# Optimization experiments

Hardware: AMD Instinct MI355X
Metric: run time of the kernel (lower is better)

Reference implementation:

```python
import jax, jax.numpy as jnp
import numpy as np

H, D_NOPE, D_ROPE, D_V, L_KV, HID = 16, 128, 64, 128, 512, 2048
D_QK = D_NOPE + D_ROPE
THETA = 10000.0
EPS = 1e-6


def _rope(x, positions):
    # neox-style rotary over last dim (D_ROPE); x: [T, ..., D_ROPE]
    half = D_ROPE // 2
    inv_freq = 1.0 / (THETA ** (jnp.arange(half, dtype=jnp.float32) * 2.0 / D_ROPE))
    ang = positions.astype(jnp.float32)[:, None] * inv_freq[None, :]  # [T, half]
    shape = (x.shape[0],) + (1,) * (x.ndim - 2) + (half,)
    cos, sin = jnp.cos(ang).reshape(shape), jnp.sin(ang).reshape(shape)
    x1, x2 = x[..., :half], x[..., half:]
    return jnp.concatenate([x1 * cos - x2 * sin, x2 * cos + x1 * sin], axis=-1)


def _rmsnorm(x, w):
    var = jnp.mean(x * x, axis=-1, keepdims=True)
    return x * jax.lax.rsqrt(var + EPS) * w


def setup_inputs() -> dict:
    key = jax.random.key(0)
    ks = jax.random.split(key, 6)
    T = 4096
    s = lambda fan_in: 1.0 / np.sqrt(fan_in)
    return {
        "positions": jnp.arange(T, dtype=jnp.int32),
        "hidden_states": jax.random.normal(ks[0], (T, HID), jnp.float32),
        "Wq": jax.random.normal(ks[1], (HID, H * D_QK), jnp.float32) * s(HID),
        "Wkva": jax.random.normal(ks[2], (HID, L_KV + D_ROPE), jnp.float32) * s(HID),
        "kv_a_ln_w": jnp.ones((L_KV,), jnp.float32),
        "Wkvb": jax.random.normal(ks[3], (L_KV, H * (D_NOPE + D_V)), jnp.float32) * s(L_KV),
        "Wo": jax.random.normal(ks[4], (H * D_V, HID), jnp.float32) * s(H * D_V),
    }


def reference(positions, hidden_states, Wq, Wkva, kv_a_ln_w, Wkvb, Wo):
    T = hidden_states.shape[0]
    scaling = 1.0 / np.sqrt(D_QK)

    q = (hidden_states @ Wq).reshape(T, H, D_QK)
    q_nope, q_pe = q[..., :D_NOPE], q[..., D_NOPE:]

    latent = hidden_states @ Wkva                    # [T, L_KV + D_ROPE]
    kv_a = _rmsnorm(latent[:, :L_KV], kv_a_ln_w)     # [T, L_KV]
    k_pe = latent[:, L_KV:]                          # [T, D_ROPE] (shared across heads)

    kv = (kv_a @ Wkvb).reshape(T, H, D_NOPE + D_V)
    k_nope, v = kv[..., :D_NOPE], kv[..., D_NOPE:]

    q_pe = _rope(q_pe, positions)                    # [T, H, D_ROPE]
    k_pe = _rope(k_pe, positions)                    # [T, D_ROPE]

    q = jnp.concatenate([q_nope, q_pe], axis=-1)     # [T, H, D_QK]
    k = jnp.concatenate(
        [k_nope, jnp.broadcast_to(k_pe[:, None, :], (T, H, D_ROPE))], axis=-1)

    scores = jnp.einsum("thd,shd->hts", q, k) * scaling        # [H, T, T]
    causal = positions[:, None] >= positions[None, :]           # [T, T]
    scores = jnp.where(causal[None], scores, jnp.finfo(scores.dtype).min)
    attn = jax.nn.softmax(scores, axis=-1)
    out = jnp.einsum("hts,shd->thd", attn, v)                   # [T, H, D_V]
    return out.reshape(T, H * D_V) @ Wo                          # [T, HID]
```

## Files before the change

kernel.cpp:

```cpp
#include <hip/hip_runtime.h>
#include <hip/hip_bf16.h>

#define T_LEN 4096
#define HID_DIM 2048
#define NH 16
#define DNOPE 128
#define DROPE 64
#define DV 128
#define LKV 512
#define DQK 192

#define BN 64

typedef __attribute__((ext_vector_type(8))) __bf16 bf16x8;
typedef __attribute__((ext_vector_type(4))) float f32x4;
typedef __attribute__((ext_vector_type(4))) short s16x4;

__device__ __forceinline__ unsigned short f2b(float f) {
  unsigned u = __builtin_bit_cast(unsigned, f);
  unsigned r = (u + 0x7FFFu + ((u >> 16) & 1u)) >> 16;
  return (unsigned short)r;
}

#define GL2LDS16(gp, lp)                                                   \
  __builtin_amdgcn_global_load_lds(                                        \
      (const __attribute__((address_space(1))) unsigned int*)(gp),         \
      (__attribute__((address_space(3))) unsigned int*)(lp), 16, 0, 0)

#if __has_builtin(__builtin_amdgcn_mfma_f32_16x16x16bf16_1k)
#define HAVE_MFMA16 1
__device__ __forceinline__ f32x4 mfma16(s16x4 a, s16x4 b, f32x4 c) {
  return __builtin_amdgcn_mfma_f32_16x16x16bf16_1k(a, b, c, 0, 0, 0);
}
#elif __has_builtin(__builtin_amdgcn_mfma_f32_16x16x16_bf16)
#define HAVE_MFMA16 1
typedef __attribute__((ext_vector_type(4))) __bf16 bf16x4v;
__device__ __forceinline__ f32x4 mfma16(s16x4 a, s16x4 b, f32x4 c) {
  return __builtin_amdgcn_mfma_f32_16x16x16_bf16(
      __builtin_bit_cast(bf16x4v, a), __builtin_bit_cast(bf16x4v, b), c, 0, 0, 0);
}
#else
#define HAVE_MFMA16 0
#endif

__global__ void k_cvt(const float* __restrict__ in, unsigned short* __restrict__ out, int n) {
  int i = blockIdx.x * 256 + threadIdx.x;
  if (i < n) out[i] = f2b(in[i]);
}

__global__ void k_transpose_all(const float* __restrict__ Wq, const float* __restrict__ Wkva,
                                const float* __restrict__ Wkvb, const float* __restrict__ Wo,
                                unsigned short* __restrict__ WqT, unsigned short* __restrict__ WkvaT,
                                unsigned short* __restrict__ WkvbT, unsigned short* __restrict__ WoT) {
  __shared__ float t[32][33];
  int bid = blockIdx.x;
  const float* in; unsigned short* out; int R, C, bx, by;
  if (bid < 6144)      { in = Wq;   out = WqT;   R = 2048; C = 3072; bx = bid % 96;  by = bid / 96; }
  else if (bid < 7296) { int b = bid - 6144; in = Wkva; out = WkvaT; R = 2048; C = 576;  bx = b % 18;  by = b / 18; }
  else if (bid < 9344) { int b = bid - 7296; in = Wkvb; out = WkvbT; R = 512;  C = 4096; bx = b % 128; by = b / 128; }
  else                 { int b = bid - 9344; in = Wo;   out = WoT;   R = 2048; C = 2048; bx = b % 64;  by = b / 64; }
  int c0 = bx * 32, r0 = by * 32;
  int tx = threadIdx.x, ty = threadIdx.y;
#pragma unroll
  for (int k = 0; k < 4; k++)
    t[ty + 8 * k][tx] = in[(size_t)(r0 + ty + 8 * k) * C + c0 + tx];
  __syncthreads();
#pragma unroll
  for (int k = 0; k < 4; k++)
    out[(size_t)(c0 + ty + 8 * k) * R + r0 + tx] = f2b(t[tx][ty + 8 * k]);
}

#define GEMM_CORE(Aptr, Btptr, Nn, Kk, ldaa, ldbb)                                         \
  __shared__ unsigned short As[128 * 32];                                                  \
  __shared__ unsigned short Bs[128 * 32];                                                  \
  int tid = threadIdx.x;                                                                   \
  int lane = tid & 63, w = tid >> 6;                                                       \
  int quad = lane >> 4, l16 = lane & 15;                                                   \
  int wm = (w >> 1) * 64, wn = (w & 1) * 64;                                               \
  int i0 = tid, i1 = tid + 256;                                                            \
  int rA0 = i0 >> 2, rA1 = i1 >> 2;                                                        \
  int c80 = (i0 & 3) * 8, c81 = (i1 & 3) * 8;                                              \
  const unsigned short* Ag0 = (Aptr) + (size_t)(m0 + rA0) * (ldaa) + c80;                  \
  const unsigned short* Ag1 = (Aptr) + (size_t)(m0 + rA1) * (ldaa) + c81;                  \
  int bR0 = n0 + rA0; if (bR0 >= (Nn)) bR0 = (Nn) - 1;                                     \
  int bR1 = n0 + rA1; if (bR1 >= (Nn)) bR1 = (Nn) - 1;                                     \
  const unsigned short* Bg0 = (Btptr) + (size_t)bR0 * (ldbb) + c80;                        \
  const unsigned short* Bg1 = (Btptr) + (size_t)bR1 * (ldbb) + c81;                        \
  f32x4 acc[4][4] = {};                                                                    \
  for (int k0 = 0; k0 < (Kk); k0 += 32) {                                                  \
    GL2LDS16(Ag0 + k0, &As[i0 * 8]);                                                       \
    GL2LDS16(Ag1 + k0, &As[i1 * 8]);                                                       \
    GL2LDS16(Bg0 + k0, &Bs[i0 * 8]);                                                       \
    GL2LDS16(Bg1 + k0, &Bs[i1 * 8]);                                                       \
    __syncthreads();                                                                       \
    bf16x8 aF[4], bF[4];                                                                   \
    _Pragma("unroll")                                                                      \
    for (int i = 0; i < 4; i++)                                                            \
      aF[i] = *(const bf16x8*)&As[(wm + i * 16 + l16) * 32 + quad * 8];                    \
    _Pragma("unroll")                                                                      \
    for (int j = 0; j < 4; j++)                                                            \
      bF[j] = *(const bf16x8*)&Bs[(wn + j * 16 + l16) * 32 + quad * 8];                    \
    _Pragma("unroll")                                                                      \
    for (int i = 0; i < 4; i++)                                                            \
      _Pragma("unroll")                                                                    \
      for (int j = 0; j < 4; j++)                                                          \
        acc[i][j] = __builtin_amdgcn_mfma_f32_16x16x32_bf16(aF[i], bF[j], acc[i][j], 0, 0, 0); \
    __syncthreads();                                                                       \
  }                                                                                        \
  int row0 = m0 + wm + quad * 4; (void)row0;

__global__ __launch_bounds__(256) void k_gemm128(
    const unsigned short* __restrict__ A, const unsigned short* __restrict__ Bt,
    float* __restrict__ Cf, int N, int K, int lda, int ldb, int ldc) {
  int m0 = blockIdx.y * 128, n0 = blockIdx.x * 128;
  GEMM_CORE(A, Bt, N, K, lda, ldb)
#pragma unroll
  for (int i = 0; i < 4; i++)
#pragma unroll
    for (int j = 0; j < 4; j++) {
      int col = n0 + wn + j * 16 + l16;
      if (col < N)
#pragma unroll
        for (int r = 0; r < 4; r++)
          Cf[(size_t)(row0 + i * 16 + r) * ldc + col] = acc[i][j][r];
    }
}

__global__ __launch_bounds__(256) void k_gemm_proj(
    const unsigned short* __restrict__ A, const unsigned short* __restrict__ WqT,
    const unsigned short* __restrict__ WkvaT, const int* __restrict__ pos,
    unsigned short* __restrict__ Qh, float* __restrict__ latentf) {
  int bxx = blockIdx.x;
  bool iswq = bxx < 24;
  const unsigned short* Bt = iswq ? WqT : WkvaT;
  int N = iswq ? NH * DQK : (LKV + DROPE);
  int m0 = blockIdx.y * 128, n0 = (iswq ? bxx : bxx - 24) * 128;
  GEMM_CORE(A, Bt, N, HID_DIM, HID_DIM, HID_DIM)
  if (iswq) {
    const float scale = 0.07216878364870323f;
    int b64 = (n0 + wn) >> 6;
    int h = b64 / 3, rem3 = b64 - 3 * h;
    unsigned short* Qb = Qh + (size_t)h * T_LEN * DQK;
    if (rem3 < 2) {
#pragma unroll
      for (int i = 0; i < 4; i++)
#pragma unroll
        for (int r = 0; r < 4; r++) {
          int t = row0 + i * 16 + r;
#pragma unroll
          for (int j = 0; j < 4; j++)
            Qb[(size_t)t * DQK + rem3 * 64 + j * 16 + l16] = f2b(acc[i][j][r] * scale);
        }
    } else {
#pragma unroll
      for (int i = 0; i < 4; i++)
#pragma unroll
        for (int r = 0; r < 4; r++) {
          int t = row0 + i * 16 + r;
          float p = (float)pos[t];
#pragma unroll
          for (int j = 0; j < 2; j++) {
            int idx = j * 16 + l16;
            float inv = __expf((float)idx * -0.2878231366242557f);
            float sn, cs;
            __sincosf(p * inv, &sn, &cs);
            float x1 = acc[i][j][r] * scale, x2 = acc[i][j + 2][r] * scale;
            Qb[(size_t)t * DQK + DNOPE + idx]      = f2b(x1 * cs - x2 * sn);
            Qb[(size_t)t * DQK + DNOPE + 32 + idx] = f2b(x2 * cs + x1 * sn);
          }
        }
    }
  } else {
#pragma unroll
    for (int i = 0; i < 4; i++)
#pragma unroll
      for (int j = 0; j < 4; j++) {
        int col = n0 + wn + j * 16 + l16;
        if (col < LKV + DROPE)
#pragma unroll
          for (int r = 0; r < 4; r++)
            latentf[(size_t)(row0 + i * 16 + r) * (LKV + DROPE) + col] = acc[i][j][r];
      }
  }
}

__global__ __launch_bounds__(256) void k_gemm_wkvb(
    const unsigned short* __restrict__ A, const unsigned short* __restrict__ Bt,
    unsigned short* __restrict__ Kh, unsigned short* __restrict__ VT) {
  int m0 = blockIdx.y * 128, n0 = blockIdx.x * 128;
  GEMM_CORE(A, Bt, NH * 256, LKV, LKV, LKV)
#pragma unroll
  for (int i = 0; i < 4; i++)
#pragma unroll
    for (int j = 0; j < 4; j++) {
      int col = n0 + wn + j * 16 + l16;
      int h = col >> 8, c = col & 255;
#pragma unroll
      for (int r = 0; r < 4; r++) {
        int t = row0 + i * 16 + r;
        unsigned short v = f2b(acc[i][j][r]);
        if (c < 128) Kh[((size_t)h * T_LEN + t) * DQK + c] = v;
        else         VT[((size_t)(h * 128 + c - 128)) * T_LEN + t] = v;
      }
    }
}

__global__ __launch_bounds__(256) void k_prep_latent(
    const float* __restrict__ latent, const float* __restrict__ w,
    const int* __restrict__ pos,
    unsigned short* __restrict__ kva, unsigned short* __restrict__ Kh) {
  __shared__ float red[256];
  int t = blockIdx.x;
  const float* row = latent + (size_t)t * (LKV + DROPE);
  float ss = 0.f;
  for (int c = threadIdx.x; c < LKV; c += 256) { float v = row[c]; ss += v * v; }
  red[threadIdx.x] = ss;
  __syncthreads();
  for (int s = 128; s > 0; s >>= 1) {
    if (threadIdx.x < s) red[threadIdx.x] += red[threadIdx.x + s];
    __syncthreads();
  }
  float rs = rsqrtf(red[0] / (float)LKV + 1e-6f);
  for (int c = threadIdx.x; c < LKV; c += 256)
    kva[(size_t)t * LKV + c] = f2b(row[c] * rs * w[c]);
  if (threadIdx.x < DROPE) {
    int i = threadIdx.x;
    float p = (float)pos[t];
    float val;
    if (i < 32) {
      float x1 = row[LKV + i], x2 = row[LKV + i + 32];
      float inv = __expf(-(float)i * 0.2878231366242557f);
      float sn, cs; __sincosf(p * inv, &sn, &cs);
      val = x1 * cs - x2 * sn;
    } else {
      float x1 = row[LKV + i - 32], x2 = row[LKV + i];
      float inv = __expf(-(float)(i - 32) * 0.2878231366242557f);
      float sn, cs; __sincosf(p * inv, &sn, &cs);
      val = x2 * cs + x1 * sn;
    }
    unsigned short vb = f2b(val);
#pragma unroll
    for (int h = 0; h < NH; h++)
      Kh[((size_t)h * T_LEN + t) * DQK + DNOPE + i] = vb;
  }
}

__global__ __launch_bounds__(256, 2) void k_flash(
    const unsigned short* __restrict__ Qh, const unsigned short* __restrict__ Kh,
    const unsigned short* __restrict__ VT, unsigned short* __restrict__ attn) {
  int bx = blockIdx.x;
  int h = bx & 15;
  int t = (bx & 255) >> 4;
  int qb = (bx < 256) ? (31 - t) : t;
  int m0 = qb * 128;
  int diagA = 2 * qb, diagB = 2 * qb + 1;
  int NT = 2 * qb + 2;

  __shared__ unsigned short Ks[64 * 24 * 8];
  __shared__ unsigned short Vs[128 * 8 * 8];

  int tid = threadIdx.x, lane = tid & 63, w = tid >> 6;
  int quad = lane >> 4, l16 = lane & 15;
  int x = l16 & 7;

  const unsigned short* Qbase = Qh + (size_t)h * T_LEN * DQK;
  const unsigned short* Kbase = Kh + (size_t)h * T_LEN * DQK;
  const unsigned short* Vbase = VT + (size_t)h * DV * T_LEN;

  bf16x8 qfS[6], qfL[6];
#pragma unroll
  for (int kk = 0; kk < 6; kk++) {
    qfS[kk] = *(const bf16x8*)(Qbase + (size_t)(m0 + w * 16 + l16) * DQK + kk * 32 + quad * 8);
    qfL[kk] = *(const bf16x8*)(Qbase + (size_t)(m0 + 64 + w * 16 + l16) * DQK + kk * 32 + quad * 8);
  }

  int koff[6], voff[4];
#pragma unroll
  for (int k = 0; k < 6; k++) {
    int c = tid + k * 256;
    int row = c / 24, sc = c - row * 24;
    int cg = (sc & 0x18) | ((sc ^ row) & 7);
    koff[k] = row * DQK + cg * 8;
  }
#pragma unroll
  for (int k = 0; k < 4; k++) {
    int c = tid + k * 256;
    int row = c >> 3, sc = c & 7;
    int cg = sc ^ (row & 7);
    voff[k] = row * T_LEN + cg * 8;
  }

  int kEo[4], kOo[4], vAo[4];
#pragma unroll
  for (int st = 0; st < 4; st++) {
    int rb = (st * 16 + l16) * 192;
    kEo[st] = rb + ((quad ^ x) * 8);
    kOo[st] = rb + (((quad + 4) ^ x) * 8);
    vAo[st] = l16 * 64 + (((st * 2 + (quad >> 1)) ^ x) * 8) + (quad & 1) * 4;
  }

  f32x4 OaccS[8] = {}, OaccL[8] = {};
  float liS = 0.f, liL = 0.f;
  int mS = m0 + w * 16 + l16;
  int mL = mS + 64;

#if !HAVE_MFMA16
  int lA = l16 + ((quad & 1) << 5);
  int lB = lA + 16;
  bool lowq = (quad < 2);
  int vFo[2];
#pragma unroll
  for (int u = 0; u < 2; u++)
    vFo[u] = l16 * 64 + (((u * 4 + quad) ^ x) * 8);
#endif

  for (int j = 0; j < NT; ++j) {
#pragma unroll
    for (int k = 0; k < 6; k++) GL2LDS16(Kbase + koff[k], &Ks[(tid + k * 256) * 8]);
#pragma unroll
    for (int k = 0; k < 4; k++) GL2LDS16(Vbase + voff[k], &Vs[(tid + k * 256) * 8]);
#pragma unroll
    for (int k = 0; k < 6; k++) koff[k] += BN * DQK;
#pragma unroll
    for (int k = 0; k < 4; k++) voff[k] += BN;
    __syncthreads();

    f32x4 ScS[4] = {}, ScL[4] = {};
#pragma unroll
    for (int kk = 0; kk < 6; kk++) {
#pragma unroll
      for (int st = 0; st < 4; st++) {
        bf16x8 kb = *(const bf16x8*)(Ks + ((kk & 1) ? kOo[st] : kEo[st]) + (kk >> 1) * 64);
        ScS[st] = __builtin_amdgcn_mfma_f32_16x16x32_bf16(kb, qfS[kk], ScS[st], 0, 0, 0);
        ScL[st] = __builtin_amdgcn_mfma_f32_16x16x32_bf16(kb, qfL[kk], ScL[st], 0, 0, 0);
      }
    }

    int n0 = j * BN;
    if (j >= diagA) {
#pragma unroll
      for (int st = 0; st < 4; st++)
#pragma unroll
        for (int r = 0; r < 4; r++) {
          int s = n0 + st * 16 + quad * 4 + r;
          if (s > mS) ScS[st][r] = -1e30f;
        }
    }
    if (j == diagB) {
#pragma unroll
      for (int st = 0; st < 4; st++)
#pragma unroll
        for (int r = 0; r < 4; r++) {
          int s = n0 + st * 16 + quad * 4 + r;
          if (s > mL) ScL[st][r] = -1e30f;
        }
    }

    unsigned p0S[4], p1S[4], p0L[4], p1L[4];
#pragma unroll
    for (int st = 0; st < 4; st++) {
      float e0 = __expf(ScS[st][0]);
      float e1 = __expf(ScS[st][1]);
      float e2 = __expf(ScS[st][2]);
      float e3 = __expf(ScS[st][3]);
      liS += (e0 + e1) + (e2 + e3);
      p0S[st] = __builtin_amdgcn_perm(__builtin_bit_cast(unsigned, e1),
                                      __builtin_bit_cast(unsigned, e0), 0x07060302u);
      p1S[st] = __builtin_amdgcn_perm(__builtin_bit_cast(unsigned, e3),
                                      __builtin_bit_cast(unsigned, e2), 0x07060302u);
      float f0 = __expf(ScL[st][0]);
      float f1 = __expf(ScL[st][1]);
      float f2 = __expf(ScL[st][2]);
      float f3 = __expf(ScL[st][3]);
      liL += (f0 + f1) + (f2 + f3);
      p0L[st] = __builtin_amdgcn_perm(__builtin_bit_cast(unsigned, f1),
                                      __builtin_bit_cast(unsigned, f0), 0x07060302u);
      p1L[st] = __builtin_amdgcn_perm(__builtin_bit_cast(unsigned, f3),
                                      __builtin_bit_cast(unsigned, f2), 0x07060302u);
    }

#if HAVE_MFMA16
#pragma unroll
    for (int st = 0; st < 4; st++) {
      uint2 puS; puS.x = p0S[st]; puS.y = p1S[st];
      s16x4 pbS = __builtin_bit_cast(s16x4, puS);
      uint2 puL; puL.x = p0L[st]; puL.y = p1L[st];
      s16x4 pbL = __builtin_bit_cast(s16x4, puL);
#pragma unroll
      for (int dt = 0; dt < 8; dt++) {
        s16x4 va = __builtin_bit_cast(s16x4, *(const uint2*)(Vs + vAo[st] + dt * 1024));
        OaccS[dt] = mfma16(va, pbS, OaccS[dt]);
        OaccL[dt] = mfma16(va, pbL, OaccL[dt]);
      }
    }
#else
#pragma unroll
    for (int u = 0; u < 2; u++) {
      int a0 = __shfl((int)p0S[2 * u], lA, 64);
      int a1 = __shfl((int)p0S[2 * u + 1], lA, 64);
      int b0 = __shfl((int)p1S[2 * u], lA, 64);
      int b1 = __shfl((int)p1S[2 * u + 1], lA, 64);
      int c0 = __shfl((int)p0S[2 * u], lB, 64);
      int c1 = __shfl((int)p0S[2 * u + 1], lB, 64);
      int d0 = __shfl((int)p1S[2 * u], lB, 64);
      int d1 = __shfl((int)p1S[2 * u + 1], lB, 64);
      int4 pkS;
      pkS.x = lowq ? a0 : a1; pkS.y = lowq ? b0 : b1;
      pkS.z = lowq ? c0 : c1; pkS.w = lowq ? d0 : d1;
      bf16x8 pbS = __builtin_bit_cast(bf16x8, pkS);
      int sa0 = __shfl((int)p0L[2 * u], lA, 64);
      int sa1 = __shfl((int)p0L[2 * u + 1], lA, 64);
      int sb0 = __shfl((int)p1L[2 * u], lA, 64);
      int sb1 = __shfl((int)p1L[2 * u + 1], lA, 64);
      int sc0 = __shfl((int)p0L[2 * u], lB, 64);
      int sc1 = __shfl((int)p0L[2 * u + 1], lB, 64);
      int sd0 = __shfl((int)p1L[2 * u], lB, 64);
      int sd1 = __shfl((int)p1L[2 * u + 1], lB, 64);
      int4 pkL;
      pkL.x = lowq ? sa0 : sa1; pkL.y = lowq ? sb0 : sb1;
      pkL.z = lowq ? sc0 : sc1; pkL.w = lowq ? sd0 : sd1;
      bf16x8 pbL = __builtin_bit_cast(bf16x8, pkL);
#pragma unroll
      for (int dt = 0; dt < 8; dt++) {
        bf16x8 va = *(const bf16x8*)(Vs + vFo[u] + dt * 1024);
        OaccS[dt] = __builtin_amdgcn_mfma_f32_16x16x32_bf16(va, pbS, OaccS[dt], 0, 0, 0);
        OaccL[dt] = __builtin_amdgcn_mfma_f32_16x16x32_bf16(va, pbL, OaccL[dt], 0, 0, 0);
      }
    }
#endif
    __syncthreads();
  }

  liS += __shfl_xor(liS, 16, 64);
  liS += __shfl_xor(liS, 32, 64);
  liL += __shfl_xor(liL, 16, 64);
  liL += __shfl_xor(liL, 32, 64);

  float invS = 1.f / liS;
  float invL = 1.f / liL;
  unsigned short* dstS = attn + (size_t)mS * HID_DIM + h * DV + quad * 4;
  unsigned short* dstL = attn + (size_t)mL * HID_DIM + h * DV + quad * 4;
#pragma unroll
  for (int dt = 0; dt < 8; dt++) {
    unsigned lo = (unsigned)f2b(OaccS[dt][0] * invS) |
                  ((unsigned)f2b(OaccS[dt][1] * invS) << 16);
    unsigned hi = (unsigned)f2b(OaccS[dt][2] * invS) |
                  ((unsigned)f2b(OaccS[dt][3] * invS) << 16);
    uint2 pkv = {lo, hi};
    *(uint2*)(dstS + dt * 16) = pkv;
    unsigned lo2 = (unsigned)f2b(OaccL[dt][0] * invL) |
                   ((unsigned)f2b(OaccL[dt][1] * invL) << 16);
    unsigned hi2 = (unsigned)f2b(OaccL[dt][2] * invL) |
                   ((unsigned)f2b(OaccL[dt][3] * invL) << 16);
    uint2 pkv2 = {lo2, hi2};
    *(uint2*)(dstL + dt * 16) = pkv2;
  }
}

extern "C" void kernel_launch(void* const* d_in, const int* in_sizes, int n_in,
                              void* d_out, int out_size, void* d_ws, size_t ws_size,
                              hipStream_t stream) {
  const int*   positions = (const int*)d_in[0];
  const float* hs   = (const float*)d_in[1];
  const float* Wq   = (const float*)d_in[2];
  const float* Wkva = (const float*)d_in[3];
  const float* lnw  = (const float*)d_in[4];
  const float* Wkvb = (const float*)d_in[5];
  const float* Wo   = (const float*)d_in[6];
  float* out = (float*)d_out;

  char* p = (char*)d_ws;
  size_t off = 0;
  auto alloc = [&](size_t bytes) {
    char* r = p + off;
    off = (off + bytes + 255) & ~(size_t)255;
    return r;
  };
  unsigned short* hsb     = (unsigned short*)alloc((size_t)T_LEN * HID_DIM * 2);
  unsigned short* WqT     = (unsigned short*)alloc((size_t)(NH * DQK) * HID_DIM * 2);
  unsigned short* WkvaT   = (unsigned short*)alloc((size_t)(LKV + DROPE) * HID_DIM * 2);
  unsigned short* WkvbT   = (unsigned short*)alloc((size_t)(NH * 256) * LKV * 2);
  unsigned short* WoT     = (unsigned short*)alloc((size_t)HID_DIM * HID_DIM * 2);
  unsigned short* Qh      = (unsigned short*)alloc((size_t)NH * T_LEN * DQK * 2);
  unsigned short* kva     = (unsigned short*)alloc((size_t)T_LEN * LKV * 2);
  unsigned short* Kh      = (unsigned short*)alloc((size_t)NH * T_LEN * DQK * 2);
  unsigned short* VT      = (unsigned short*)alloc((size_t)NH * DV * T_LEN * 2);
  unsigned short* attn    = (unsigned short*)alloc((size_t)T_LEN * HID_DIM * 2);
  float*          latentf = (float*)alloc((size_t)T_LEN * (LKV + DROPE) * 4);

  k_cvt<<<(T_LEN * HID_DIM + 255) / 256, 256, 0, stream>>>(hs, hsb, T_LEN * HID_DIM);
  k_transpose_all<<<13440, dim3(32, 8), 0, stream>>>(Wq, Wkva, Wkvb, Wo, WqT, WkvaT, WkvbT, WoT);

  k_gemm_proj<<<dim3(29, T_LEN / 128), 256, 0, stream>>>(hsb, WqT, WkvaT, positions, Qh, latentf);

  k_prep_latent<<<T_LEN, 256, 0, stream>>>(latentf, lnw, positions, kva, Kh);

  k_gemm_wkvb<<<dim3((NH * 256) / 128, T_LEN / 128), 256, 0, stream>>>(kva, WkvbT, Kh, VT);

  k_flash<<<dim3(512), 256, 0, stream>>>(Qh, Kh, VT, attn);

  k_gemm128<<<dim3(HID_DIM / 128, T_LEN / 128), 256, 0, stream>>>(
      attn, WoT, out, HID_DIM, HID_DIM, HID_DIM, HID_DIM, HID_DIM);
}
```

Measured before the change: 500.7 us.

## Double-buffer K/V shared-memory tiles in flash attention kernel

Allocates two LDS buffers for the K and V tiles and issues the global-to-LDS loads for the next tile before computing on the current one. The per-iteration pair of barriers becomes one vmcnt wait plus barrier at the end of each iteration. This is meant to hide global load latency behind MFMA work. It doubles LDS use per block, which could limit occupancy if LDS capacity is tight.

New measurement: 499.6 us. About the same (-0.2%).

```diff
diff --git a/kernel.cpp b/kernel.cpp
--- a/kernel.cpp
+++ b/kernel.cpp
@@ -256,8 +256,8 @@
   int diagA = 2 * qb, diagB = 2 * qb + 1;
   int NT = 2 * qb + 2;
 
-  __shared__ unsigned short Ks[64 * 24 * 8];
-  __shared__ unsigned short Vs[128 * 8 * 8];
+  __shared__ unsigned short Ks[2 * 64 * 24 * 8];
+  __shared__ unsigned short Vs[2 * 128 * 8 * 8];
 
   int tid = threadIdx.x, lane = tid & 63, w = tid >> 6;
   int quad = lane >> 4, l16 = lane & 15;
@@ -314,23 +314,43 @@
     vFo[u] = l16 * 64 + (((u * 4 + quad) ^ x) * 8);
 #endif
 
+#define STAGE(buf)                                                                         \
+  do {                                                                                     \
+    unsigned short* ksd = Ks + (buf) * (64 * 24 * 8);                                      \
+    unsigned short* vsd = Vs + (buf) * (128 * 8 * 8);                                      \
+    _Pragma("unroll")                                                                      \
+    for (int k = 0; k < 6; k++) GL2LDS16(Kbase + koff[k], &ksd[(tid + k * 256) * 8]);      \
+    _Pragma("unroll")                                                                      \
+    for (int k = 0; k < 4; k++) GL2LDS16(Vbase + voff[k], &vsd[(tid + k * 256) * 8]);      \
+    _Pragma("unroll")                                                                      \
+    for (int k = 0; k < 6; k++) koff[k] += BN * DQK;                                       \
+    _Pragma("unroll")                                                                      \
+    for (int k = 0; k < 4; k++) voff[k] += BN;                                             \
+  } while (0)
+
+#define PIPE_BARRIER()                                                                     \
+  do {                                                                                     \
+    asm volatile("s_waitcnt vmcnt(0)" ::: "memory");                                       \
+    __builtin_amdgcn_s_barrier();                                                          \
+    __builtin_amdgcn_sched_barrier(0);                                                     \
+  } while (0)
+
+  STAGE(0);
+  PIPE_BARRIER();
+
+  int cur = 0;
   for (int j = 0; j < NT; ++j) {
-#pragma unroll
-    for (int k = 0; k < 6; k++) GL2LDS16(Kbase + koff[k], &Ks[(tid + k * 256) * 8]);
-#pragma unroll
-    for (int k = 0; k < 4; k++) GL2LDS16(Vbase + voff[k], &Vs[(tid + k * 256) * 8]);
-#pragma unroll
-    for (int k = 0; k < 6; k++) koff[k] += BN * DQK;
-#pragma unroll
-    for (int k = 0; k < 4; k++) voff[k] += BN;
-    __syncthreads();
+    if (j + 1 < NT) STAGE(cur ^ 1);
+
+    const unsigned short* KsB = Ks + cur * (64 * 24 * 8);
+    const unsigned short* VsB = Vs + cur * (128 * 8 * 8);
 
     f32x4 ScS[4] = {}, ScL[4] = {};
 #pragma unroll
     for (int kk = 0; kk < 6; kk++) {
 #pragma unroll
       for (int st = 0; st < 4; st++) {
-        bf16x8 kb = *(const bf16x8*)(Ks + ((kk & 1) ? kOo[st] : kEo[st]) + (kk >> 1) * 64);
+        bf16x8 kb = *(const bf16x8*)(KsB + ((kk & 1) ? kOo[st] : kEo[st]) + (kk >> 1) * 64);
         ScS[st] = __builtin_amdgcn_mfma_f32_16x16x32_bf16(kb, qfS[kk], ScS[st], 0, 0, 0);
         ScL[st] = __builtin_amdgcn_mfma_f32_16x16x32_bf16(kb, qfL[kk], ScL[st], 0, 0, 0);
       }
@@ -388,7 +408,7 @@
       s16x4 pbL = __builtin_bit_cast(s16x4, puL);
 #pragma unroll
       for (int dt = 0; dt < 8; dt++) {
-        s16x4 va = __builtin_bit_cast(s16x4, *(const uint2*)(Vs + vAo[st] + dt * 1024));
+        s16x4 va = __builtin_bit_cast(s16x4, *(const uint2*)(VsB + vAo[st] + dt * 1024));
         OaccS[dt] = mfma16(va, pbS, OaccS[dt]);
         OaccL[dt] = mfma16(va, pbL, OaccL[dt]);
       }
@@ -422,13 +442,15 @@
       bf16x8 pbL = __builtin_bit_cast(bf16x8, pkL);
 #pragma unroll
       for (int dt = 0; dt < 8; dt++) {
-        bf16x8 va = *(const bf16x8*)(Vs + vFo[u] + dt * 1024);
+        bf16x8 va = *(const bf16x8*)(VsB + vFo[u] + dt * 1024);
         OaccS[dt] = __builtin_amdgcn_mfma_f32_16x16x32_bf16(va, pbS, OaccS[dt], 0, 0, 0);
         OaccL[dt] = __builtin_amdgcn_mfma_f32_16x16x32_bf16(va, pbL, OaccL[dt], 0, 0, 0);
       }
     }
 #endif
-    __syncthreads();
+
+    PIPE_BARRIER();
+    cur ^= 1;
   }
 
   liS += __shfl_xor(liS, 16, 64);
@@ -455,6 +477,8 @@
     uint2 pkv2 = {lo2, hi2};
     *(uint2*)(dstL + dt * 16) = pkv2;
   }
+#undef STAGE
+#undef PIPE_BARRIER
 }
 
 extern "C" void kernel_launch(void* const* d_in, const int* in_sizes, int n_in,
```
